# Performance work log

Hardware: AMD Instinct MI355X
Metric: run time of the kernel (lower is better)

The kernel has to match this reference:

```python
import jax, jax.numpy as jnp
import numpy as np

N = 2_000_000

def setup_inputs() -> dict:
    key = jax.random.key(0)
    k1, k2 = jax.random.split(key)
    # means spread so a realistic mix lies inside and outside the unit sphere
    means = jax.random.normal(k1, (N, 3), dtype=jnp.float32) * 2.0
    # symmetric PSD covariances (like real ray-sample Gaussians)
    A = jax.random.normal(k2, (N, 3, 3), dtype=jnp.float32) * 0.1
    cov = jnp.einsum('nij,nkj->nik', A, A)
    return {"means": means, "cov": cov}

def _contract(x):
    # f(x) = x if ||x||<=1 else (2 - 1/||x||) * x/||x||   (Frobenius / L2 norm)
    mag = jnp.linalg.norm(x, axis=-1, keepdims=True)
    return jnp.where(mag < 1, x, (2 - 1 / mag) * (x / mag))

def _contract_gauss(x):
    # single point version used for Jacobian (applied everywhere, as in torch source)
    n = jnp.linalg.norm(x)
    return (2 - 1 / n) * (x / n)

def reference(means, cov):
    new_means = _contract(means)
    # per-point 3x3 Jacobian via autodiff, mirroring vmap(jacrev(...)) in torch
    jc = jax.vmap(jax.jacrev(_contract_gauss))(means)  # [N,3,3]
    mag = jnp.linalg.norm(means, axis=-1)              # [N]
    mask = mag >= 1
    # J @ cov @ J^T for contracted points
    new_cov = jnp.einsum('nij,njk,nlk->nil', jc, cov, jc)  # [N,3,3]
    cov_out = jnp.where(mask[:, None, None], new_cov, cov)
    return new_means, cov_out
```

## Files before the change

### kernel.cpp

```cpp
#include <hip/hip_runtime.h>


#define BLOCK 256

__global__ __launch_bounds__(BLOCK) void scene_contraction_kernel(
    const float* __restrict__ means,
    const float* __restrict__ cov,
    float* __restrict__ out_means,
    float* __restrict__ out_cov,
    int n)
{
    __shared__ float sm[BLOCK * 3];
    __shared__ float sc[BLOCK * 9];

    const int t  = threadIdx.x;
    const long p0 = (long)blockIdx.x * BLOCK;
    const int npts = (int)min((long)BLOCK, (long)n - p0);
    if (npts <= 0) return;

    {
        const int nf = 3 * npts;
        const int nq = nf >> 2;
        const float4* g4 = (const float4*)(means + 3L * p0);
        float4* s4 = (float4*)sm;
        for (int q = t; q < nq; q += BLOCK) s4[q] = g4[q];
        for (int r = (nq << 2) + t; r < nf; r += BLOCK) sm[r] = means[3L * p0 + r];
    }
    {
        const int nf = 9 * npts;
        const int nq = nf >> 2;
        const float4* g4 = (const float4*)(cov + 9L * p0);
        float4* s4 = (float4*)sc;
        for (int q = t; q < nq; q += BLOCK) s4[q] = g4[q];
        for (int r = (nq << 2) + t; r < nf; r += BLOCK) sc[r] = cov[9L * p0 + r];
    }
    __syncthreads();

    const bool active = (t < npts);
    float ox=0, oy=0, oz=0;
    float t00=0,t01=0,t02=0,t10=0,t11=0,t12=0,t20=0,t21=0,t22=0;

    if (active) {
        const float x = sm[3*t + 0];
        const float y = sm[3*t + 1];
        const float z = sm[3*t + 2];

        const float c00 = sc[9*t + 0];
        const float c01 = sc[9*t + 1];
        const float c02 = sc[9*t + 2];
        const float c10 = sc[9*t + 3];
        const float c11 = sc[9*t + 4];
        const float c12 = sc[9*t + 5];
        const float c20 = sc[9*t + 6];
        const float c21 = sc[9*t + 7];
        const float c22 = sc[9*t + 8];

        const float n2 = x*x + y*y + z*z;
        const bool inside = (n2 < 1.0f);

        const float nrm = sqrtf(n2);
        const float inv = 1.0f / nrm;
        const float f   = (2.0f - inv) * inv;
        const float s   = (2.0f * nrm - 1.0f) * inv * inv;
        const float c   = 2.0f * (1.0f - nrm) / (n2 * n2);

        ox = inside ? x : f * x;
        oy = inside ? y : f * y;
        oz = inside ? z : f * z;

        const float u0 = c00*x + c01*y + c02*z;
        const float u1 = c10*x + c11*y + c12*z;
        const float u2 = c20*x + c21*y + c22*z;
        const float q  = x*u0 + y*u1 + z*u2;

        const float s2  = s * s;
        const float scc = s * c;
        const float c2q = c * c * q;

        t00 = inside ? c00 : s2*c00 + scc*(u0*x + x*u0) + c2q*x*x;
        t01 = inside ? c01 : s2*c01 + scc*(u0*y + x*u1) + c2q*x*y;
        t02 = inside ? c02 : s2*c02 + scc*(u0*z + x*u2) + c2q*x*z;
        t10 = inside ? c10 : s2*c10 + scc*(u1*x + y*u0) + c2q*y*x;
        t11 = inside ? c11 : s2*c11 + scc*(u1*y + y*u1) + c2q*y*y;
        t12 = inside ? c12 : s2*c12 + scc*(u1*z + y*u2) + c2q*y*z;
        t20 = inside ? c20 : s2*c20 + scc*(u2*x + z*u0) + c2q*z*x;
        t21 = inside ? c21 : s2*c21 + scc*(u2*y + z*u1) + c2q*z*y;
        t22 = inside ? c22 : s2*c22 + scc*(u2*z + z*u2) + c2q*z*z;
    }
    __syncthreads();

    if (active) {
        sm[3*t + 0] = ox;  sm[3*t + 1] = oy;  sm[3*t + 2] = oz;
        sc[9*t + 0] = t00; sc[9*t + 1] = t01; sc[9*t + 2] = t02;
        sc[9*t + 3] = t10; sc[9*t + 4] = t11; sc[9*t + 5] = t12;
        sc[9*t + 6] = t20; sc[9*t + 7] = t21; sc[9*t + 8] = t22;
    }
    __syncthreads();

    {
        const int nf = 3 * npts;
        const int nq = nf >> 2;
        float4* g4 = (float4*)(out_means + 3L * p0);
        const float4* s4 = (const float4*)sm;
        for (int q = t; q < nq; q += BLOCK) g4[q] = s4[q];
        for (int r = (nq << 2) + t; r < nf; r += BLOCK) out_means[3L * p0 + r] = sm[r];
    }
    {
        const int nf = 9 * npts;
        const int nq = nf >> 2;
        float4* g4 = (float4*)(out_cov + 9L * p0);
        const float4* s4 = (const float4*)sc;
        for (int q = t; q < nq; q += BLOCK) g4[q] = s4[q];
        for (int r = (nq << 2) + t; r < nf; r += BLOCK) out_cov[9L * p0 + r] = sc[r];
    }
}

extern "C" void kernel_launch(void* const* d_in, const int* in_sizes, int n_in,
                              void* d_out, int out_size, void* d_ws, size_t ws_size,
                              hipStream_t stream) {
    const float* means = (const float*)d_in[0];
    const float* cov   = (const float*)d_in[1];
    const int n = in_sizes[0] / 3;

    float* out_means = (float*)d_out;
    float* out_cov   = (float*)d_out + (size_t)n * 3;

    const int grid = (n + BLOCK - 1) / BLOCK;
    hipLaunchKernelGGL(scene_contraction_kernel, dim3(grid), dim3(BLOCK), 0, stream,
                       means, cov, out_means, out_cov, n);
}
```

Measured before the change: 34.89 us.

## Process four points per thread with direct float4 loads, dropping shared-memory staging

Each thread now handles a group of four points, loading 3 float4 of means and 9 float4 of covariance straight from global memory into registers, computing in registers, and writing float4 results back. This removes the shared-memory round trip and the three block barriers of the old staging scheme. In exchange, each thread's float4 accesses are strided by 48 or 144 bytes, so a wavefront's loads are less contiguous. The grid also shrinks by four times and per-thread register use rises. A single thread handles the leftover points when n is not a multiple of four.

```diff
diff --git a/kernel.cpp b/kernel.cpp
--- a/kernel.cpp
+++ b/kernel.cpp
@@ -3,115 +3,119 @@
 
 #define BLOCK 256
 
-__global__ __launch_bounds__(BLOCK) void scene_contraction_kernel(
+__device__ __forceinline__ void contract_one(
+    float x, float y, float z,
+    float c00, float c01, float c02,
+    float c10, float c11, float c12,
+    float c20, float c21, float c22,
+    float& ox, float& oy, float& oz,
+    float& t00, float& t01, float& t02,
+    float& t10, float& t11, float& t12,
+    float& t20, float& t21, float& t22)
+{
+    const float n2 = x*x + y*y + z*z;
+    const bool inside = (n2 < 1.0f);
+
+    const float nrm = sqrtf(n2);
+    const float inv = 1.0f / nrm;
+    const float f   = (2.0f - inv) * inv;
+    const float s   = (2.0f * nrm - 1.0f) * inv * inv;
+    const float c   = 2.0f * (1.0f - nrm) / (n2 * n2);
+
+    ox = inside ? x : f * x;
+    oy = inside ? y : f * y;
+    oz = inside ? z : f * z;
+
+    const float u0 = c00*x + c01*y + c02*z;
+    const float u1 = c10*x + c11*y + c12*z;
+    const float u2 = c20*x + c21*y + c22*z;
+    const float q  = x*u0 + y*u1 + z*u2;
+
+    const float s2  = s * s;
+    const float scc = s * c;
+    const float c2q = c * c * q;
+
+    t00 = inside ? c00 : s2*c00 + scc*(u0*x + x*u0) + c2q*x*x;
+    t01 = inside ? c01 : s2*c01 + scc*(u0*y + x*u1) + c2q*x*y;
+    t02 = inside ? c02 : s2*c02 + scc*(u0*z + x*u2) + c2q*x*z;
+    t10 = inside ? c10 : s2*c10 + scc*(u1*x + y*u0) + c2q*y*x;
+    t11 = inside ? c11 : s2*c11 + scc*(u1*y + y*u1) + c2q*y*y;
+    t12 = inside ? c12 : s2*c12 + scc*(u1*z + y*u2) + c2q*y*z;
+    t20 = inside ? c20 : s2*c20 + scc*(u2*x + z*u0) + c2q*z*x;
+    t21 = inside ? c21 : s2*c21 + scc*(u2*y + z*u1) + c2q*z*y;
+    t22 = inside ? c22 : s2*c22 + scc*(u2*z + z*u2) + c2q*z*z;
+}
+
+__global__ __launch_bounds__(BLOCK) void scene_contraction4_kernel(
+    const float4* __restrict__ m4,
+    const float4* __restrict__ c4,
+    float4* __restrict__ om4,
+    float4* __restrict__ oc4,
     const float* __restrict__ means,
     const float* __restrict__ cov,
     float* __restrict__ out_means,
     float* __restrict__ out_cov,
-    int n)
+    int ngroups, int n)
 {
-    __shared__ float sm[BLOCK * 3];
-    __shared__ float sc[BLOCK * 9];
+    const int g = blockIdx.x * blockDim.x + threadIdx.x;
 
-    const int t  = threadIdx.x;
-    const long p0 = (long)blockIdx.x * BLOCK;
-    const int npts = (int)min((long)BLOCK, (long)n - p0);
-    if (npts <= 0) return;
+    if (g < ngroups) {
+        const size_t mb = 3 * (size_t)g;
+        const size_t cb = 9 * (size_t)g;
 
-    {
-        const int nf = 3 * npts;
-        const int nq = nf >> 2;
-        const float4* g4 = (const float4*)(means + 3L * p0);
-        float4* s4 = (float4*)sm;
-        for (int q = t; q < nq; q += BLOCK) s4[q] = g4[q];
-        for (int r = (nq << 2) + t; r < nf; r += BLOCK) sm[r] = means[3L * p0 + r];
-    }
-    {
-        const int nf = 9 * npts;
-        const int nq = nf >> 2;
-        const float4* g4 = (const float4*)(cov + 9L * p0);
-        float4* s4 = (float4*)sc;
-        for (int q = t; q < nq; q += BLOCK) s4[q] = g4[q];
-        for (int r = (nq << 2) + t; r < nf; r += BLOCK) sc[r] = cov[9L * p0 + r];
-    }
-    __syncthreads();
+        const float4 Ma = m4[mb + 0];
+        const float4 Mb = m4[mb + 1];
+        const float4 Mc = m4[mb + 2];
+        const float4 Ca = c4[cb + 0];
+        const float4 Cb = c4[cb + 1];
+        const float4 Cc = c4[cb + 2];
+        const float4 Cd = c4[cb + 3];
+        const float4 Ce = c4[cb + 4];
+        const float4 Cf = c4[cb + 5];
+        const float4 Cg = c4[cb + 6];
+        const float4 Ch = c4[cb + 7];
+        const float4 Ci = c4[cb + 8];
 
-    const bool active = (t < npts);
-    float ox=0, oy=0, oz=0;
-    float t00=0,t01=0,t02=0,t10=0,t11=0,t12=0,t20=0,t21=0,t22=0;
+        const float mf[12] = {Ma.x,Ma.y,Ma.z,Ma.w, Mb.x,Mb.y,Mb.z,Mb.w, Mc.x,Mc.y,Mc.z,Mc.w};
+        const float cf[36] = {Ca.x,Ca.y,Ca.z,Ca.w, Cb.x,Cb.y,Cb.z,Cb.w, Cc.x,Cc.y,Cc.z,Cc.w,
+                              Cd.x,Cd.y,Cd.z,Cd.w, Ce.x,Ce.y,Ce.z,Ce.w, Cf.x,Cf.y,Cf.z,Cf.w,
+                              Cg.x,Cg.y,Cg.z,Cg.w, Ch.x,Ch.y,Ch.z,Ch.w, Ci.x,Ci.y,Ci.z,Ci.w};
+        float of[12], tf[36];
 
-    if (active) {
-        const float x = sm[3*t + 0];
-        const float y = sm[3*t + 1];
-        const float z = sm[3*t + 2];
+#pragma unroll
+        for (int p = 0; p < 4; ++p) {
+            contract_one(mf[3*p+0], mf[3*p+1], mf[3*p+2],
+                         cf[9*p+0], cf[9*p+1], cf[9*p+2],
+                         cf[9*p+3], cf[9*p+4], cf[9*p+5],
+                         cf[9*p+6], cf[9*p+7], cf[9*p+8],
+                         of[3*p+0], of[3*p+1], of[3*p+2],
+                         tf[9*p+0], tf[9*p+1], tf[9*p+2],
+                         tf[9*p+3], tf[9*p+4], tf[9*p+5],
+                         tf[9*p+6], tf[9*p+7], tf[9*p+8]);
+        }
 
-        const float c00 = sc[9*t + 0];
-        const float c01 = sc[9*t + 1];
-        const float c02 = sc[9*t + 2];
-        const float c10 = sc[9*t + 3];
-        const float c11 = sc[9*t + 4];
-        const float c12 = sc[9*t + 5];
-        const float c20 = sc[9*t + 6];
-        const float c21 = sc[9*t + 7];
-        const float c22 = sc[9*t + 8];
-
-        const float n2 = x*x + y*y + z*z;
-        const bool inside = (n2 < 1.0f);
-
-        const float nrm = sqrtf(n2);
-        const float inv = 1.0f / nrm;
-        const float f   = (2.0f - inv) * inv;
-        const float s   = (2.0f * nrm - 1.0f) * inv * inv;
-        const float c   = 2.0f * (1.0f - nrm) / (n2 * n2);
-
-        ox = inside ? x : f * x;
-        oy = inside ? y : f * y;
-        oz = inside ? z : f * z;
-
-        const float u0 = c00*x + c01*y + c02*z;
-        const float u1 = c10*x + c11*y + c12*z;
-        const float u2 = c20*x + c21*y + c22*z;
-        const float q  = x*u0 + y*u1 + z*u2;
-
-        const float s2  = s * s;
-        const float scc = s * c;
-        const float c2q = c * c * q;
-
-        t00 = inside ? c00 : s2*c00 + scc*(u0*x + x*u0) + c2q*x*x;
-        t01 = inside ? c01 : s2*c01 + scc*(u0*y + x*u1) + c2q*x*y;
-        t02 = inside ? c02 : s2*c02 + scc*(u0*z + x*u2) + c2q*x*z;
-        t10 = inside ? c10 : s2*c10 + scc*(u1*x + y*u0) + c2q*y*x;
-        t11 = inside ? c11 : s2*c11 + scc*(u1*y + y*u1) + c2q*y*y;
-        t12 = inside ? c12 : s2*c12 + scc*(u1*z + y*u2) + c2q*y*z;
-        t20 = inside ? c20 : s2*c20 + scc*(u2*x + z*u0) + c2q*z*x;
-        t21 = inside ? c21 : s2*c21 + scc*(u2*y + z*u1) + c2q*z*y;
-        t22 = inside ? c22 : s2*c22 + scc*(u2*z + z*u2) + c2q*z*z;
-    }
-    __syncthreads();
-
-    if (active) {
-        sm[3*t + 0] = ox;  sm[3*t + 1] = oy;  sm[3*t + 2] = oz;
-        sc[9*t + 0] = t00; sc[9*t + 1] = t01; sc[9*t + 2] = t02;
-        sc[9*t + 3] = t10; sc[9*t + 4] = t11; sc[9*t + 5] = t12;
-        sc[9*t + 6] = t20; sc[9*t + 7] = t21; sc[9*t + 8] = t22;
-    }
-    __syncthreads();
-
-    {
-        const int nf = 3 * npts;
-        const int nq = nf >> 2;
-        float4* g4 = (float4*)(out_means + 3L * p0);
-        const float4* s4 = (const float4*)sm;
-        for (int q = t; q < nq; q += BLOCK) g4[q] = s4[q];
-        for (int r = (nq << 2) + t; r < nf; r += BLOCK) out_means[3L * p0 + r] = sm[r];
-    }
-    {
-        const int nf = 9 * npts;
-        const int nq = nf >> 2;
-        float4* g4 = (float4*)(out_cov + 9L * p0);
-        const float4* s4 = (const float4*)sc;
-        for (int q = t; q < nq; q += BLOCK) g4[q] = s4[q];
-        for (int r = (nq << 2) + t; r < nf; r += BLOCK) out_cov[9L * p0 + r] = sc[r];
+        om4[mb + 0] = make_float4(of[0], of[1], of[2],  of[3]);
+        om4[mb + 1] = make_float4(of[4], of[5], of[6],  of[7]);
+        om4[mb + 2] = make_float4(of[8], of[9], of[10], of[11]);
+#pragma unroll
+        for (int k = 0; k < 9; ++k)
+            oc4[cb + k] = make_float4(tf[4*k+0], tf[4*k+1], tf[4*k+2], tf[4*k+3]);
+    } else if (g == ngroups) {
+        for (int i = 4 * ngroups; i < n; ++i) {
+            const size_t mbase = 3 * (size_t)i;
+            const size_t cbase = 9 * (size_t)i;
+            float ox, oy, oz, t00, t01, t02, t10, t11, t12, t20, t21, t22;
+            contract_one(means[mbase+0], means[mbase+1], means[mbase+2],
+                         cov[cbase+0], cov[cbase+1], cov[cbase+2],
+                         cov[cbase+3], cov[cbase+4], cov[cbase+5],
+                         cov[cbase+6], cov[cbase+7], cov[cbase+8],
+                         ox, oy, oz,
+                         t00, t01, t02, t10, t11, t12, t20, t21, t22);
+            out_means[mbase+0] = ox; out_means[mbase+1] = oy; out_means[mbase+2] = oz;
+            out_cov[cbase+0] = t00; out_cov[cbase+1] = t01; out_cov[cbase+2] = t02;
+            out_cov[cbase+3] = t10; out_cov[cbase+4] = t11; out_cov[cbase+5] = t12;
+            out_cov[cbase+6] = t20; out_cov[cbase+7] = t21; out_cov[cbase+8] = t22;
+        }
     }
 }
 
@@ -125,7 +129,14 @@
     float* out_means = (float*)d_out;
     float* out_cov   = (float*)d_out + (size_t)n * 3;
 
-    const int grid = (n + BLOCK - 1) / BLOCK;
-    hipLaunchKernelGGL(scene_contraction_kernel, dim3(grid), dim3(BLOCK), 0, stream,
-                       means, cov, out_means, out_cov, n);
+    const int ngroups = n / 4;
+    const int rem = n - 4 * ngroups;
+    const int nthreads = ngroups + (rem ? 1 : 0);
+    const int grid = (nthreads + BLOCK - 1) / BLOCK;
+
+    hipLaunchKernelGGL(scene_contraction4_kernel, dim3(grid), dim3(BLOCK), 0, stream,
+                       (const float4*)means, (const float4*)cov,
+                       (float4*)out_means, (float4*)out_cov,
+                       means, cov, out_means, out_cov,
+                       ngroups, n);
 }
```

Measured after the change: 64.32 us. +84.3%, slower.
